# Kernel tuning notes

Measured on AMD Instinct MI355X. Metric: run time of the kernel, lower is better.

## Reference

```python
import jax, jax.numpy as jnp
import numpy as np

EMBED_DIM = 1024
NUM_HEADS = 16
HEAD_DIM = EMBED_DIM // NUM_HEADS
ROPE_BASE = 10000.0


def setup_inputs() -> dict:
    key = jax.random.key(0)
    k1, k2, k3, k4, k5 = jax.random.split(key, 5)
    b, t = 4, 2048
    s = 1.0 / np.sqrt(EMBED_DIM)
    return {
        "query": jax.random.normal(k1, (b, t, EMBED_DIM), jnp.float32),
        "in_proj_w": jax.random.normal(k2, (3 * EMBED_DIM, EMBED_DIM), jnp.float32) * s,
        "in_proj_b": jax.random.normal(k3, (3 * EMBED_DIM,), jnp.float32) * 0.02,
        "out_proj_w": jax.random.normal(k4, (EMBED_DIM, EMBED_DIM), jnp.float32) * s,
        "out_proj_b": jax.random.normal(k5, (EMBED_DIM,), jnp.float32) * 0.02,
    }


def _rope_cos_sin(t: int, dtype):
    inv_freq = 1.0 / (ROPE_BASE ** (jnp.arange(0, HEAD_DIM, 2, dtype=jnp.float32) / HEAD_DIM))
    freqs = jnp.arange(t, dtype=jnp.float32)[:, None] * inv_freq[None, :]  # [t, hd/2]
    return jnp.cos(freqs).astype(dtype), jnp.sin(freqs).astype(dtype)


def _apply_rotary(x, cos, sin):
    # x: [b, h, t, hd]; cos/sin: [t, hd/2]
    x1 = x[..., ::2]
    x2 = x[..., 1::2]
    c = cos[None, None, :, :]
    s = sin[None, None, :, :]
    rotated = jnp.stack((x1 * c - x2 * s, x1 * s + x2 * c), axis=-1)  # [b,h,t,hd/2,2]
    return rotated.reshape(x.shape)


def reference(query, in_proj_w, in_proj_b, out_proj_w, out_proj_b):
    b, t, d = query.shape
    qkv = query @ in_proj_w.T + in_proj_b  # [b, t, 3d]
    q, k, v = jnp.split(qkv, 3, axis=-1)
    def heads(x):
        return x.reshape(b, t, NUM_HEADS, HEAD_DIM).transpose(0, 2, 1, 3)  # [b,h,t,hd]
    q, k, v = heads(q), heads(k), heads(v)
    cos, sin = _rope_cos_sin(t, query.dtype)
    q = _apply_rotary(q, cos, sin)
    k = _apply_rotary(k, cos, sin)
    scale = 1.0 / np.sqrt(HEAD_DIM)
    scores = jnp.einsum('bhqd,bhkd->bhqk', q, k) * scale  # [b,h,t,t]
    probs = jax.nn.softmax(scores, axis=-1)
    attn = jnp.einsum('bhqk,bhkd->bhqd', probs, v)
    out = attn.transpose(0, 2, 1, 3).reshape(b, t, d)
    return out @ out_proj_w.T + out_proj_b
```

## Files before the change

### kernel.cpp

```cpp
#include <hip/hip_runtime.h>
#include <hip/hip_bf16.h>

#define EMBED 1024
#define NHEADS 16
#define HDIM 64
#define BATCH 4
#define SEQ 2048
#define BT (BATCH*SEQ)
#define NQKV (3*EMBED)


typedef _Float16 f16;
typedef __attribute__((ext_vector_type(8))) _Float16 half8;
typedef __attribute__((ext_vector_type(4))) _Float16 half4;
typedef __attribute__((ext_vector_type(2))) __fp16 h2raw;
typedef __attribute__((ext_vector_type(4))) float f32x4;
typedef __attribute__((ext_vector_type(16))) float f32x16;
typedef __attribute__((ext_vector_type(4))) unsigned int u32x4;

#define QSCALE2 0.18033688f

__device__ __forceinline__ float fexp2(float x) {
#if __has_builtin(__builtin_amdgcn_exp2f)
    return __builtin_amdgcn_exp2f(x);
#else
    float r;
    asm("v_exp_f32 %0, %1" : "=v"(r) : "v"(x));
    return r;
#endif
}

__device__ __forceinline__ float fdot2a(unsigned int w, float c) {
#if __has_builtin(__builtin_amdgcn_fdot2)
    h2raw ones;
    ones[0] = (__fp16)1.0f; ones[1] = (__fp16)1.0f;
    return __builtin_amdgcn_fdot2(__builtin_bit_cast(h2raw, w), ones, c, false);
#else
    f16 lo = (f16)__builtin_bit_cast(h2raw, w)[0];
    f16 hi = (f16)__builtin_bit_cast(h2raw, w)[1];
    return c + (float)lo + (float)hi;
#endif
}

__device__ __forceinline__ f32x4 mfma16f(half8 a, half8 b, f32x4 c) {
    return __builtin_amdgcn_mfma_f32_16x16x32_f16(a, b, c, 0, 0, 0);
}
__device__ __forceinline__ f32x16 mfma32(half8 a, half8 b, f32x16 c) {
    return __builtin_amdgcn_mfma_f32_32x32x16_f16(a, b, c, 0, 0, 0);
}
__device__ __forceinline__ f32x16 z16() {
    f32x16 z;
    #pragma unroll
    for (int i = 0; i < 16; i++) z[i] = 0.f;
    return z;
}
__device__ __forceinline__ unsigned int pk16(float a, float b) {
    auto h = __builtin_amdgcn_cvt_pkrtz(a, b);
    return __builtin_bit_cast(unsigned int, h);
}
__device__ __forceinline__ half8 mk8(unsigned int w0, unsigned int w1,
                                     unsigned int w2, unsigned int w3) {
    u32x4 v = (u32x4){w0, w1, w2, w3};
    return __builtin_bit_cast(half8, v);
}
__device__ __forceinline__ void pswap(unsigned int &a, unsigned int &b) {
    asm("v_permlane32_swap_b32 %0, %1" : "+v"(a), "+v"(b));
}

__device__ __forceinline__ half8 cvt8(float4 a, float4 b) {
    half8 r;
    r[0] = (f16)a.x; r[1] = (f16)a.y; r[2] = (f16)a.z; r[3] = (f16)a.w;
    r[4] = (f16)b.x; r[5] = (f16)b.y; r[6] = (f16)b.z; r[7] = (f16)b.w;
    return r;
}

__device__ __forceinline__ void gload16(const void* g, void* l) {
    __builtin_amdgcn_global_load_lds(
        (const __attribute__((address_space(1))) void*)g,
        (__attribute__((address_space(3))) void*)l, 16, 0, 0);
}

__global__ __launch_bounds__(256) void cvt_kernel(
    const float* __restrict__ X, const float* __restrict__ W1,
    const float* __restrict__ W2, f16* __restrict__ Xh,
    f16* __restrict__ W1h, f16* __restrict__ W2h, float2* __restrict__ CSt)
{
    const int u0 = blockIdx.x * 256 + threadIdx.x;
    #pragma unroll
    for (int i = 0; i < 3; i++) {
        const size_t uu = (size_t)u0 + (size_t)i * 524288;
        const float* src; f16* dst; size_t off;
        if (uu < 1048576)      { src = X;  dst = Xh;  off = uu * 8; }
        else if (uu < 1441792) { src = W1; dst = W1h; off = (uu - 1048576) * 8; }
        else                   { src = W2; dst = W2h; off = (uu - 1441792) * 8; }
        float4 a = *(const float4*)(src + off);
        float4 b = *(const float4*)(src + off + 4);
        *(half8*)(dst + off) = cvt8(a, b);
    }
    if (u0 < SEQ * 32) {
        const int t = u0 >> 5, fi = u0 & 31;
        const float ang = (float)t * exp2f(-0.41524103f * (float)fi);
        CSt[u0] = make_float2(cosf(ang), sinf(ang));
    }
}

__global__ __launch_bounds__(512, 4) void qkv_rope_kernel(
    const f16* __restrict__ Xh, const f16* __restrict__ Wh,
    const float* __restrict__ bias, const float2* __restrict__ CSt,
    f16* __restrict__ Qg, f16* __restrict__ Kg, f16* __restrict__ Vtg)
{
    __shared__ __align__(16) char smem[65536];
    f16* A0 = (f16*)smem;
    f16* B0 = (f16*)(smem + 16384);
    f16* A1 = (f16*)(smem + 32768);
    f16* B1 = (f16*)(smem + 49152);
    f16 (*Ep)[136] = (f16(*)[136])smem;

    const int tid = threadIdx.x;

    const int lin = blockIdx.y * 24 + blockIdx.x;
    const int xcd = lin & 7;
    const int c   = lin >> 3;
    const int m0  = (xcd * 8 + (c & 7)) * 128;
    const int n0  = (c >> 3) * 128;

    const int lane = tid & 63;
    const int wv = tid >> 6;
    const int wm = wv >> 2, wn = wv & 3;
    const int quad = lane >> 4, l15 = lane & 15;
    const int sw = (l15 & 7) << 4;

    const int rlo   = tid >> 3;
    const int sslot = (tid & 7) ^ (rlo & 7);
    const f16* asrc = Xh + (size_t)(m0 + rlo) * EMBED + sslot * 8;
    const f16* bsrc = Wh + (size_t)(n0 + rlo) * EMBED + sslot * 8;

    f32x4 acc[4][2];
    #pragma unroll
    for (int i = 0; i < 4; i++)
        #pragma unroll
        for (int j = 0; j < 2; j++) acc[i][j] = (f32x4){0.f,0.f,0.f,0.f};

    gload16(asrc,                      A0 + tid*8);
    gload16(asrc + (size_t)64*EMBED,   A0 + 4096 + tid*8);
    gload16(bsrc,                      B0 + tid*8);
    gload16(bsrc + (size_t)64*EMBED,   B0 + 4096 + tid*8);
    __syncthreads();

    for (int t = 0; t < 16; t++) {
        const f16* Ac = (t & 1) ? A1 : A0;
        const f16* Bc = (t & 1) ? B1 : B0;
        if (t < 15) {
            f16* An = (t & 1) ? A0 : A1;
            f16* Bn = (t & 1) ? B0 : B1;
            const int k0 = (t + 1) * 64;
            gload16(asrc + k0,                    An + tid*8);
            gload16(asrc + (size_t)64*EMBED + k0, An + 4096 + tid*8);
            gload16(bsrc + k0,                    Bn + tid*8);
            gload16(bsrc + (size_t)64*EMBED + k0, Bn + 4096 + tid*8);
        }

        half8 bf[2][2];
        #pragma unroll
        for (int nj = 0; nj < 2; nj++) {
            const int rb = wn*32 + nj*16 + l15;
            bf[nj][0] = *(const half8*)((const char*)Bc + rb*128 + ((quad*16) ^ sw));
            bf[nj][1] = *(const half8*)((const char*)Bc + rb*128 + ((64 + quad*16) ^ sw));
        }
        #pragma unroll
        for (int mi = 0; mi < 4; mi++) {
            const int ra = wm*64 + mi*16 + l15;
            half8 a0 = *(const half8*)((const char*)Ac + ra*128 + ((quad*16) ^ sw));
            half8 a1 = *(const half8*)((const char*)Ac + ra*128 + ((64 + quad*16) ^ sw));
            #pragma unroll
            for (int nj = 0; nj < 2; nj++) {
                acc[mi][nj] = mfma16f(a0, bf[nj][0], acc[mi][nj]);
                acc[mi][nj] = mfma16f(a1, bf[nj][1], acc[mi][nj]);
            }
        }
        __syncthreads();
    }

    const int sect = n0 >> 10;
    const int h0   = (n0 & 1023) >> 6;
    const int bb   = m0 >> 11, t0 = m0 & 2047;

    #pragma unroll
    for (int mi = 0; mi < 4; mi++) {
        #pragma unroll
        for (int nj = 0; nj < 2; nj++) {
            const int ncol = wn*32 + nj*16 + l15;
            const int hd = ncol & 63;
            const float bz = bias[n0 + ncol];
            #pragma unroll
            for (int r = 0; r < 4; r++) {
                const int tl = wm*64 + mi*16 + quad*4 + r;
                float v = acc[mi][nj][r] + bz;
                if (sect < 2) {
                    float partner = __shfl_xor(v, 1, 64);
                    float2 cs2 = CSt[(t0 + tl)*32 + (hd >> 1)];
                    float o = (hd & 1) ? fmaf(partner, cs2.y, v * cs2.x)
                                       : fmaf(v, cs2.x, -(partner * cs2.y));
                    if (sect == 0) o *= QSCALE2;
                    Ep[tl][ncol] = (f16)o;
                } else {
                    Ep[ncol][tl] = (f16)v;
                }
            }
        }
    }
    __syncthreads();

    const int orow = tid >> 2;
    const int oc   = (tid & 3) * 32;
    f16* dst;
    if (sect == 2) {
        const int h = h0 + (orow >> 6), d = orow & 63;
        dst = Vtg + ((size_t)((bb*NHEADS + h) * HDIM + d)) * SEQ + t0 + oc;
    } else {
        const int h = h0 + (oc >> 6);
        f16* base = (sect == 0) ? Qg : Kg;
        dst = base + ((size_t)((bb*NHEADS + h) * SEQ + t0 + orow)) * HDIM + (oc & 63);
    }
    #pragma unroll
    for (int c8 = 0; c8 < 4; c8++)
        *(half8*)(dst + c8*8) = *(const half8*)&Ep[orow][oc + c8*8];
}

__global__ __launch_bounds__(256, 2) void attn_kernel(
    const f16* __restrict__ Qg, const f16* __restrict__ Kg,
    const f16* __restrict__ Vtg, f16* __restrict__ Ow)
{
    __shared__ __align__(16) f16 KV[2][2][64*64];

    const int tid  = threadIdx.x;
    const int lane = tid & 63, wq = tid >> 6;
    const int hi   = lane >> 5, col = lane & 31;

    const int lin = blockIdx.y * 8 + blockIdx.x;
    const int bh  = (lin & 7) + ((lin >> 6) << 3);
    const int qb  = (lin >> 3) & 7;
    const int q0  = qb * 256;

    const f16* Kb = Kg  + (size_t)bh * SEQ * HDIM;
    const f16* Vb = Vtg + (size_t)bh * HDIM * SEQ;

    const int r8   = tid >> 3;
    const int slot = tid & 7;

    #pragma unroll
    for (int g = 0; g < 2; g++) {
        const int row = g*32 + r8;
        const int sc  = (slot ^ (row & 7)) * 8;
        gload16(Kb + (size_t)row * HDIM + sc, &KV[0][0][0] + g*2048 + tid*8);
        gload16(Vb + (size_t)row * SEQ  + sc, &KV[0][1][0] + g*2048 + tid*8);
    }

    half8 qf[2][4];
    #pragma unroll
    for (int nb = 0; nb < 2; nb++) {
        const f16* qsrc = Qg + (size_t)bh * SEQ * HDIM
                        + (size_t)(q0 + wq*64 + nb*32 + col) * HDIM + hi*8;
        #pragma unroll
        for (int kc = 0; kc < 4; kc++)
            qf[nb][kc] = *(const half8*)(qsrc + kc*16);
    }

    f32x16 oacc[2][2];
    oacc[0][0] = z16(); oacc[0][1] = z16();
    oacc[1][0] = z16(); oacc[1][1] = z16();
    float lsA[2] = {0.f, 0.f};
    float lsB[2] = {0.f, 0.f};

    __syncthreads();

    for (int it = 0; it < 32; it++) {
        const f16* kl = &KV[it & 1][0][0];
        const f16* vl = &KV[it & 1][1][0];

        if (it < 31) {
            f16* kd = &KV[(it + 1) & 1][0][0];
            f16* vd = &KV[(it + 1) & 1][1][0];
            const int j0n = (it + 1) * 64;
            #pragma unroll
            for (int g = 0; g < 2; g++) {
                const int row = g*32 + r8;
                const int sc  = (slot ^ (row & 7)) * 8;
                gload16(Kb + (size_t)(j0n + row) * HDIM + sc, kd + g*2048 + tid*8);
                gload16(Vb + (size_t)row * SEQ + j0n + sc,    vd + g*2048 + tid*8);
            }
        }

        half8 kf[2][4];
        #pragma unroll
        for (int jb = 0; jb < 2; jb++) {
            const int row = jb*32 + col;
            const char* base = (const char*)kl + row*128;
            const int sz = (row & 7) << 4;
            #pragma unroll
            for (int kc = 0; kc < 4; kc++)
                kf[jb][kc] = *(const half8*)(base + ((kc*32 + hi*16) ^ sz));
        }

        unsigned int pw[2][4][4];
        #pragma unroll
        for (int nb = 0; nb < 2; nb++) {
            f32x16 s0 = z16(), s1 = z16();
            __builtin_amdgcn_s_setprio(1);
            #pragma unroll
            for (int kc = 0; kc < 4; kc++) s0 = mfma32(kf[0][kc], qf[nb][kc], s0);
            #pragma unroll
            for (int kc = 0; kc < 4; kc++) s1 = mfma32(kf[1][kc], qf[nb][kc], s1);
            __builtin_amdgcn_s_setprio(0);

            float e0[16], e1[16];
            #pragma unroll
            for (int r = 0; r < 16; r++) {
                e0[r] = fexp2(s0[r]);
                e1[r] = fexp2(s1[r]);
            }

            unsigned int a, b;
            a = pk16(e0[0],  e0[1]);  b = pk16(e0[4],  e0[5]);
            lsA[nb] = fdot2a(a, lsA[nb]); lsB[nb] = fdot2a(b, lsB[nb]);
            pswap(a, b); pw[nb][0][0] = a; pw[nb][0][2] = b;
            a = pk16(e0[2],  e0[3]);  b = pk16(e0[6],  e0[7]);
            lsA[nb] = fdot2a(a, lsA[nb]); lsB[nb] = fdot2a(b, lsB[nb]);
            pswap(a, b); pw[nb][0][1] = a; pw[nb][0][3] = b;
            a = pk16(e0[8],  e0[9]);  b = pk16(e0[12], e0[13]);
            lsA[nb] = fdot2a(a, lsA[nb]); lsB[nb] = fdot2a(b, lsB[nb]);
            pswap(a, b); pw[nb][1][0] = a; pw[nb][1][2] = b;
            a = pk16(e0[10], e0[11]); b = pk16(e0[14], e0[15]);
            lsA[nb] = fdot2a(a, lsA[nb]); lsB[nb] = fdot2a(b, lsB[nb]);
            pswap(a, b); pw[nb][1][1] = a; pw[nb][1][3] = b;

            a = pk16(e1[0],  e1[1]);  b = pk16(e1[4],  e1[5]);
            lsA[nb] = fdot2a(a, lsA[nb]); lsB[nb] = fdot2a(b, lsB[nb]);
            pswap(a, b); pw[nb][2][0] = a; pw[nb][2][2] = b;
            a = pk16(e1[2],  e1[3]);  b = pk16(e1[6],  e1[7]);
            lsA[nb] = fdot2a(a, lsA[nb]); lsB[nb] = fdot2a(b, lsB[nb]);
            pswap(a, b); pw[nb][2][1] = a; pw[nb][2][3] = b;
            a = pk16(e1[8],  e1[9]);  b = pk16(e1[12], e1[13]);
            lsA[nb] = fdot2a(a, lsA[nb]); lsB[nb] = fdot2a(b, lsB[nb]);
            pswap(a, b); pw[nb][3][0] = a; pw[nb][3][2] = b;
            a = pk16(e1[10], e1[11]); b = pk16(e1[14], e1[15]);
            lsA[nb] = fdot2a(a, lsA[nb]); lsB[nb] = fdot2a(b, lsB[nb]);
            pswap(a, b); pw[nb][3][1] = a; pw[nb][3][3] = b;
        }

        __builtin_amdgcn_s_setprio(1);
        #pragma unroll
        for (int kc2 = 0; kc2 < 4; kc2++) {
            half8 pb0 = mk8(pw[0][kc2][0], pw[0][kc2][1], pw[0][kc2][2], pw[0][kc2][3]);
            half8 pb1 = mk8(pw[1][kc2][0], pw[1][kc2][1], pw[1][kc2][2], pw[1][kc2][3]);
            #pragma unroll
            for (int db = 0; db < 2; db++) {
                const int row = db*32 + col;
                const int sz = (row & 7) << 4;
                half8 vf = *(const half8*)((const char*)vl + row*128
                                           + ((kc2*32 + hi*16) ^ sz));
                oacc[db][0] = mfma32(vf, pb0, oacc[db][0]);
                oacc[db][1] = mfma32(vf, pb1, oacc[db][1]);
            }
        }
        __builtin_amdgcn_s_setprio(0);

        __syncthreads();
    }

    float invl[2];
    {
        float l0 = lsA[0] + lsB[0];
        float l1 = lsA[1] + lsB[1];
        invl[0] = 1.0f / (l0 + __shfl_xor(l0, 32, 64));
        invl[1] = 1.0f / (l1 + __shfl_xor(l1, 32, 64));
    }

    const int bb = bh >> 4, h = bh & 15;
    #pragma unroll
    for (int nb = 0; nb < 2; nb++) {
        const int t = q0 + wq*64 + nb*32 + col;
        f16* od = Ow + (size_t)(bb*SEQ + t) * EMBED + h*HDIM + hi*4;
        #pragma unroll
        for (int db = 0; db < 2; db++) {
            #pragma unroll
            for (int rg = 0; rg < 4; rg++) {
                half4 o;
                o[0] = (f16)(oacc[db][nb][rg*4+0] * invl[nb]);
                o[1] = (f16)(oacc[db][nb][rg*4+1] * invl[nb]);
                o[2] = (f16)(oacc[db][nb][rg*4+2] * invl[nb]);
                o[3] = (f16)(oacc[db][nb][rg*4+3] * invl[nb]);
                *(half4*)(od + db*32 + rg*8) = o;
            }
        }
    }
}

__global__ __launch_bounds__(512, 4) void outproj_kernel(
    const f16* __restrict__ Aw, const f16* __restrict__ Wh,
    const float* __restrict__ bias, float* __restrict__ Out)
{
    __shared__ __align__(16) char smem[65536];
    f16* A0 = (f16*)smem;
    f16* B0 = (f16*)(smem + 16384);
    f16* A1 = (f16*)(smem + 32768);
    f16* B1 = (f16*)(smem + 49152);

    const int tid = threadIdx.x;

    const int lin = blockIdx.y * 8 + blockIdx.x;
    const int xcd = lin & 7;
    const int c   = lin >> 3;
    const int m0  = (xcd * 8 + (c & 7)) * 128;
    const int n0  = (c >> 3) * 128;

    const int lane = tid & 63;
    const int wv = tid >> 6;
    const int wm = wv >> 2, wn = wv & 3;
    const int quad = lane >> 4, l15 = lane & 15;
    const int sw = (l15 & 7) << 4;

    const int rlo   = tid >> 3;
    const int sslot = (tid & 7) ^ (rlo & 7);
    const f16* asrc = Aw + (size_t)(m0 + rlo) * EMBED + sslot * 8;
    const f16* bsrc = Wh + (size_t)(n0 + rlo) * EMBED + sslot * 8;

    f32x4 acc[4][2];
    #pragma unroll
    for (int i = 0; i < 4; i++)
        #pragma unroll
        for (int j = 0; j < 2; j++) acc[i][j] = (f32x4){0.f,0.f,0.f,0.f};

    gload16(asrc,                      A0 + tid*8);
    gload16(asrc + (size_t)64*EMBED,   A0 + 4096 + tid*8);
    gload16(bsrc,                      B0 + tid*8);
    gload16(bsrc + (size_t)64*EMBED,   B0 + 4096 + tid*8);
    __syncthreads();

    for (int t = 0; t < 16; t++) {
        const f16* Ac = (t & 1) ? A1 : A0;
        const f16* Bc = (t & 1) ? B1 : B0;
        if (t < 15) {
            f16* An = (t & 1) ? A0 : A1;
            f16* Bn = (t & 1) ? B0 : B1;
            const int k0 = (t + 1) * 64;
            gload16(asrc + k0,                    An + tid*8);
            gload16(asrc + (size_t)64*EMBED + k0, An + 4096 + tid*8);
            gload16(bsrc + k0,                    Bn + tid*8);
            gload16(bsrc + (size_t)64*EMBED + k0, Bn + 4096 + tid*8);
        }

        half8 bf[2][2];
        #pragma unroll
        for (int nj = 0; nj < 2; nj++) {
            const int rb = wn*32 + nj*16 + l15;
            bf[nj][0] = *(const half8*)((const char*)Bc + rb*128 + ((quad*16) ^ sw));
            bf[nj][1] = *(const half8*)((const char*)Bc + rb*128 + ((64 + quad*16) ^ sw));
        }
        #pragma unroll
        for (int mi = 0; mi < 4; mi++) {
            const int ra = wm*64 + mi*16 + l15;
            half8 a0 = *(const half8*)((const char*)Ac + ra*128 + ((quad*16) ^ sw));
            half8 a1 = *(const half8*)((const char*)Ac + ra*128 + ((64 + quad*16) ^ sw));
            #pragma unroll
            for (int nj = 0; nj < 2; nj++) {
                acc[mi][nj] = mfma16f(a0, bf[nj][0], acc[mi][nj]);
                acc[mi][nj] = mfma16f(a1, bf[nj][1], acc[mi][nj]);
            }
        }
        __syncthreads();
    }

    #pragma unroll
    for (int mi = 0; mi < 4; mi++) {
        #pragma unroll
        for (int nj = 0; nj < 2; nj++) {
            const int n = n0 + wn*32 + nj*16 + l15;
            const float bz = bias[n];
            #pragma unroll
            for (int r = 0; r < 4; r++) {
                const int m = m0 + wm*64 + mi*16 + quad*4 + r;
                Out[(size_t)m * EMBED + n] = acc[mi][nj][r] + bz;
            }
        }
    }
}

extern "C" void kernel_launch(void* const* d_in, const int* in_sizes, int n_in,
                              void* d_out, int out_size, void* d_ws, size_t ws_size,
                              hipStream_t stream)
{
    const float* query = (const float*)d_in[0];
    const float* in_w  = (const float*)d_in[1];
    const float* in_b  = (const float*)d_in[2];
    const float* out_w = (const float*)d_in[3];
    const float* out_b = (const float*)d_in[4];
    float* out = (float*)d_out;

    const size_t NT = (size_t)BATCH * NHEADS * SEQ * HDIM;
    char* ws = (char*)d_ws;
    f16* Qg  = (f16*)ws;
    f16* Kg  = (f16*)(ws + 2*NT);
    f16* Vtg = (f16*)(ws + 4*NT);
    f16* Aw  = (f16*)(ws + 6*NT);
    f16* Xh  = (f16*)(ws + 6*NT);
    f16* W1h = (f16*)(ws + 8*NT);
    f16* W2h = (f16*)(ws + 8*NT + 6291456);
    float2* CSt = (float2*)(ws + 8*NT + 6291456 + 2097152);

    cvt_kernel<<<2048, 256, 0, stream>>>(query, in_w, out_w, Xh, W1h, W2h, CSt);
    dim3 g1(NQKV / 128, BT / 128);
    qkv_rope_kernel<<<g1, 512, 0, stream>>>(Xh, W1h, in_b, CSt, Qg, Kg, Vtg);
    dim3 g2(SEQ / 256, BATCH * NHEADS);
    attn_kernel<<<g2, 256, 0, stream>>>(Qg, Kg, Vtg, Aw);
    dim3 g3(EMBED / 128, BT / 128);
    outproj_kernel<<<g3, 512, 0, stream>>>(Aw, W2h, out_b, out);
}
```

Measured before the change: 290.4 us.

## Switch projection GEMMs to 32x32 MFMA with 4 waves and single-buffered LDS

Both projection GEMMs (QKV+RoPE and output) move from 8-wave blocks issuing 16x16x32 MFMAs to 4-wave blocks where each wave computes a 64x64 tile with 32x32x16 MFMAs. The LDS double buffer is dropped in favour of one A/B buffer loaded and consumed each k-step, and the epilogue and store indexing are remapped to the 32x32 accumulator layout. Larger MFMA tiles cut LDS fragment reads per flop and the smaller LDS footprint may allow more resident blocks. The cost is that global-load latency is no longer overlapped with compute within a block.

Measured after the change: 279.2 us. 1.04x faster.

```diff
diff --git a/kernel.cpp b/kernel.cpp
--- a/kernel.cpp
+++ b/kernel.cpp
@@ -42,9 +42,6 @@
 #endif
 }
 
-__device__ __forceinline__ f32x4 mfma16f(half8 a, half8 b, f32x4 c) {
-    return __builtin_amdgcn_mfma_f32_16x16x32_f16(a, b, c, 0, 0, 0);
-}
 __device__ __forceinline__ f32x16 mfma32(half8 a, half8 b, f32x16 c) {
     return __builtin_amdgcn_mfma_f32_32x32x16_f16(a, b, c, 0, 0, 0);
 }
@@ -104,16 +101,14 @@
     }
 }
 
-__global__ __launch_bounds__(512, 4) void qkv_rope_kernel(
+__global__ __launch_bounds__(256, 4) void qkv_rope_kernel(
     const f16* __restrict__ Xh, const f16* __restrict__ Wh,
     const float* __restrict__ bias, const float2* __restrict__ CSt,
     f16* __restrict__ Qg, f16* __restrict__ Kg, f16* __restrict__ Vtg)
 {
-    __shared__ __align__(16) char smem[65536];
-    f16* A0 = (f16*)smem;
-    f16* B0 = (f16*)(smem + 16384);
-    f16* A1 = (f16*)(smem + 32768);
-    f16* B1 = (f16*)(smem + 49152);
+    __shared__ __align__(16) char smem[34816];
+    f16* Ah = (f16*)smem;
+    f16* Bh = (f16*)(smem + 16384);
     f16 (*Ep)[136] = (f16(*)[136])smem;
 
     const int tid = threadIdx.x;
@@ -126,57 +121,42 @@
 
     const int lane = tid & 63;
     const int wv = tid >> 6;
-    const int wm = wv >> 2, wn = wv & 3;
-    const int quad = lane >> 4, l15 = lane & 15;
-    const int sw = (l15 & 7) << 4;
+    const int wm = wv >> 1, wn = wv & 1;
+    const int hi = lane >> 5, col = lane & 31;
 
     const int rlo   = tid >> 3;
     const int sslot = (tid & 7) ^ (rlo & 7);
     const f16* asrc = Xh + (size_t)(m0 + rlo) * EMBED + sslot * 8;
     const f16* bsrc = Wh + (size_t)(n0 + rlo) * EMBED + sslot * 8;
 
-    f32x4 acc[4][2];
-    #pragma unroll
-    for (int i = 0; i < 4; i++)
-        #pragma unroll
-        for (int j = 0; j < 2; j++) acc[i][j] = (f32x4){0.f,0.f,0.f,0.f};
-
-    gload16(asrc,                      A0 + tid*8);
-    gload16(asrc + (size_t)64*EMBED,   A0 + 4096 + tid*8);
-    gload16(bsrc,                      B0 + tid*8);
-    gload16(bsrc + (size_t)64*EMBED,   B0 + 4096 + tid*8);
-    __syncthreads();
-
-    for (int t = 0; t < 16; t++) {
-        const f16* Ac = (t & 1) ? A1 : A0;
-        const f16* Bc = (t & 1) ? B1 : B0;
-        if (t < 15) {
-            f16* An = (t & 1) ? A0 : A1;
-            f16* Bn = (t & 1) ? B0 : B1;
-            const int k0 = (t + 1) * 64;
-            gload16(asrc + k0,                    An + tid*8);
-            gload16(asrc + (size_t)64*EMBED + k0, An + 4096 + tid*8);
-            gload16(bsrc + k0,                    Bn + tid*8);
-            gload16(bsrc + (size_t)64*EMBED + k0, Bn + 4096 + tid*8);
-        }
-
-        half8 bf[2][2];
-        #pragma unroll
-        for (int nj = 0; nj < 2; nj++) {
-            const int rb = wn*32 + nj*16 + l15;
-            bf[nj][0] = *(const half8*)((const char*)Bc + rb*128 + ((quad*16) ^ sw));
-            bf[nj][1] = *(const half8*)((const char*)Bc + rb*128 + ((64 + quad*16) ^ sw));
-        }
-        #pragma unroll
-        for (int mi = 0; mi < 4; mi++) {
-            const int ra = wm*64 + mi*16 + l15;
-            half8 a0 = *(const half8*)((const char*)Ac + ra*128 + ((quad*16) ^ sw));
-            half8 a1 = *(const half8*)((const char*)Ac + ra*128 + ((64 + quad*16) ^ sw));
-            #pragma unroll
-            for (int nj = 0; nj < 2; nj++) {
-                acc[mi][nj] = mfma16f(a0, bf[nj][0], acc[mi][nj]);
-                acc[mi][nj] = mfma16f(a1, bf[nj][1], acc[mi][nj]);
-            }
+    const int ra0 = wm*64 + col,      ra1 = wm*64 + 32 + col;
+    const int rb0 = wn*64 + col,      rb1 = wn*64 + 32 + col;
+    const int sza0 = (ra0 & 7) << 4,  sza1 = (ra1 & 7) << 4;
+    const int szb0 = (rb0 & 7) << 4,  szb1 = (rb1 & 7) << 4;
+
+    f32x16 acc[2][2];
+    acc[0][0] = z16(); acc[0][1] = z16();
+    acc[1][0] = z16(); acc[1][1] = z16();
+
+    for (int k0 = 0; k0 < EMBED; k0 += 64) {
+        #pragma unroll
+        for (int i = 0; i < 4; i++) {
+            gload16(asrc + (size_t)i*32*EMBED + k0, Ah + i*2048 + tid*8);
+            gload16(bsrc + (size_t)i*32*EMBED + k0, Bh + i*2048 + tid*8);
+        }
+        __syncthreads();
+
+        #pragma unroll
+        for (int ks = 0; ks < 4; ks++) {
+            const int ko = ks*32 + hi*16;
+            half8 a0 = *(const half8*)((const char*)Ah + ra0*128 + (ko ^ sza0));
+            half8 a1 = *(const half8*)((const char*)Ah + ra1*128 + (ko ^ sza1));
+            half8 b0 = *(const half8*)((const char*)Bh + rb0*128 + (ko ^ szb0));
+            half8 b1 = *(const half8*)((const char*)Bh + rb1*128 + (ko ^ szb1));
+            acc[0][0] = mfma32(a0, b0, acc[0][0]);
+            acc[0][1] = mfma32(a0, b1, acc[0][1]);
+            acc[1][0] = mfma32(a1, b0, acc[1][0]);
+            acc[1][1] = mfma32(a1, b1, acc[1][1]);
         }
         __syncthreads();
     }
@@ -186,16 +166,16 @@
     const int bb   = m0 >> 11, t0 = m0 & 2047;
 
     #pragma unroll
-    for (int mi = 0; mi < 4; mi++) {
-        #pragma unroll
-        for (int nj = 0; nj < 2; nj++) {
-            const int ncol = wn*32 + nj*16 + l15;
+    for (int mb = 0; mb < 2; mb++) {
+        #pragma unroll
+        for (int nbk = 0; nbk < 2; nbk++) {
+            const int ncol = wn*64 + nbk*32 + col;
             const int hd = ncol & 63;
             const float bz = bias[n0 + ncol];
             #pragma unroll
-            for (int r = 0; r < 4; r++) {
-                const int tl = wm*64 + mi*16 + quad*4 + r;
-                float v = acc[mi][nj][r] + bz;
+            for (int reg = 0; reg < 16; reg++) {
+                const int tl = wm*64 + mb*32 + (reg & 3) + 8*(reg >> 2) + 4*hi;
+                float v = acc[mb][nbk][reg] + bz;
                 if (sect < 2) {
                     float partner = __shfl_xor(v, 1, 64);
                     float2 cs2 = CSt[(t0 + tl)*32 + (hd >> 1)];
@@ -211,19 +191,19 @@
     }
     __syncthreads();
 
-    const int orow = tid >> 2;
-    const int oc   = (tid & 3) * 32;
+    const int orow = tid >> 1;
+    const int oc   = (tid & 1) * 64;
     f16* dst;
     if (sect == 2) {
         const int h = h0 + (orow >> 6), d = orow & 63;
         dst = Vtg + ((size_t)((bb*NHEADS + h) * HDIM + d)) * SEQ + t0 + oc;
     } else {
-        const int h = h0 + (oc >> 6);
+        const int h = h0 + (tid & 1);
         f16* base = (sect == 0) ? Qg : Kg;
-        dst = base + ((size_t)((bb*NHEADS + h) * SEQ + t0 + orow)) * HDIM + (oc & 63);
-    }
-    #pragma unroll
-    for (int c8 = 0; c8 < 4; c8++)
+        dst = base + ((size_t)((bb*NHEADS + h) * SEQ + t0 + orow)) * HDIM;
+    }
+    #pragma unroll
+    for (int c8 = 0; c8 < 8; c8++)
         *(half8*)(dst + c8*8) = *(const half8*)&Ep[orow][oc + c8*8];
 }
 
@@ -396,15 +376,13 @@
     }
 }
 
-__global__ __launch_bounds__(512, 4) void outproj_kernel(
+__global__ __launch_bounds__(256, 4) void outproj_kernel(
     const f16* __restrict__ Aw, const f16* __restrict__ Wh,
     const float* __restrict__ bias, float* __restrict__ Out)
 {
-    __shared__ __align__(16) char smem[65536];
-    f16* A0 = (f16*)smem;
-    f16* B0 = (f16*)(smem + 16384);
-    f16* A1 = (f16*)(smem + 32768);
-    f16* B1 = (f16*)(smem + 49152);
+    __shared__ __align__(16) char smem[32768];
+    f16* Ah = (f16*)smem;
+    f16* Bh = (f16*)(smem + 16384);
 
     const int tid = threadIdx.x;
 
@@ -416,71 +394,56 @@
 
     const int lane = tid & 63;
     const int wv = tid >> 6;
-    const int wm = wv >> 2, wn = wv & 3;
-    const int quad = lane >> 4, l15 = lane & 15;
-    const int sw = (l15 & 7) << 4;
+    const int wm = wv >> 1, wn = wv & 1;
+    const int hi = lane >> 5, col = lane & 31;
 
     const int rlo   = tid >> 3;
     const int sslot = (tid & 7) ^ (rlo & 7);
     const f16* asrc = Aw + (size_t)(m0 + rlo) * EMBED + sslot * 8;
     const f16* bsrc = Wh + (size_t)(n0 + rlo) * EMBED + sslot * 8;
 
-    f32x4 acc[4][2];
-    #pragma unroll
-    for (int i = 0; i < 4; i++)
-        #pragma unroll
-        for (int j = 0; j < 2; j++) acc[i][j] = (f32x4){0.f,0.f,0.f,0.f};
-
-    gload16(asrc,                      A0 + tid*8);
-    gload16(asrc + (size_t)64*EMBED,   A0 + 4096 + tid*8);
-    gload16(bsrc,                      B0 + tid*8);
-    gload16(bsrc + (size_t)64*EMBED,   B0 + 4096 + tid*8);
-    __syncthreads();
-
-    for (int t = 0; t < 16; t++) {
-        const f16* Ac = (t & 1) ? A1 : A0;
-        const f16* Bc = (t & 1) ? B1 : B0;
-        if (t < 15) {
-            f16* An = (t & 1) ? A0 : A1;
-            f16* Bn = (t & 1) ? B0 : B1;
-            const int k0 = (t + 1) * 64;
-            gload16(asrc + k0,                    An + tid*8);
-            gload16(asrc + (size_t)64*EMBED + k0, An + 4096 + tid*8);
-            gload16(bsrc + k0,                    Bn + tid*8);
-            gload16(bsrc + (size_t)64*EMBED + k0, Bn + 4096 + tid*8);
-        }
-
-        half8 bf[2][2];
-        #pragma unroll
-        for (int nj = 0; nj < 2; nj++) {
-            const int rb = wn*32 + nj*16 + l15;
-            bf[nj][0] = *(const half8*)((const char*)Bc + rb*128 + ((quad*16) ^ sw));
-            bf[nj][1] = *(const half8*)((const char*)Bc + rb*128 + ((64 + quad*16) ^ sw));
-        }
-        #pragma unroll
-        for (int mi = 0; mi < 4; mi++) {
-            const int ra = wm*64 + mi*16 + l15;
-            half8 a0 = *(const half8*)((const char*)Ac + ra*128 + ((quad*16) ^ sw));
-            half8 a1 = *(const half8*)((const char*)Ac + ra*128 + ((64 + quad*16) ^ sw));
-            #pragma unroll
-            for (int nj = 0; nj < 2; nj++) {
-                acc[mi][nj] = mfma16f(a0, bf[nj][0], acc[mi][nj]);
-                acc[mi][nj] = mfma16f(a1, bf[nj][1], acc[mi][nj]);
-            }
+    const int ra0 = wm*64 + col,      ra1 = wm*64 + 32 + col;
+    const int rb0 = wn*64 + col,      rb1 = wn*64 + 32 + col;
+    const int sza0 = (ra0 & 7) << 4,  sza1 = (ra1 & 7) << 4;
+    const int szb0 = (rb0 & 7) << 4,  szb1 = (rb1 & 7) << 4;
+
+    f32x16 acc[2][2];
+    acc[0][0] = z16(); acc[0][1] = z16();
+    acc[1][0] = z16(); acc[1][1] = z16();
+
+    for (int k0 = 0; k0 < EMBED; k0 += 64) {
+        #pragma unroll
+        for (int i = 0; i < 4; i++) {
+            gload16(asrc + (size_t)i*32*EMBED + k0, Ah + i*2048 + tid*8);
+            gload16(bsrc + (size_t)i*32*EMBED + k0, Bh + i*2048 + tid*8);
         }
         __syncthreads();
-    }
-
-    #pragma unroll
-    for (int mi = 0; mi < 4; mi++) {
-        #pragma unroll
-        for (int nj = 0; nj < 2; nj++) {
-            const int n = n0 + wn*32 + nj*16 + l15;
+
+        #pragma unroll
+        for (int ks = 0; ks < 4; ks++) {
+            const int ko = ks*32 + hi*16;
+            half8 a0 = *(const half8*)((const char*)Ah + ra0*128 + (ko ^ sza0));
+            half8 a1 = *(const half8*)((const char*)Ah + ra1*128 + (ko ^ sza1));
+            half8 b0 = *(const half8*)((const char*)Bh + rb0*128 + (ko ^ szb0));
+            half8 b1 = *(const half8*)((const char*)Bh + rb1*128 + (ko ^ szb1));
+            acc[0][0] = mfma32(a0, b0, acc[0][0]);
+            acc[0][1] = mfma32(a0, b1, acc[0][1]);
+            acc[1][0] = mfma32(a1, b0, acc[1][0]);
+            acc[1][1] = mfma32(a1, b1, acc[1][1]);
+        }
+        __syncthreads();
+    }
+
+    #pragma unroll
+    for (int mb = 0; mb < 2; mb++) {
+        #pragma unroll
+        for (int nbk = 0; nbk < 2; nbk++) {
+            const int n = n0 + wn*64 + nbk*32 + col;
             const float bz = bias[n];
             #pragma unroll
-            for (int r = 0; r < 4; r++) {
-                const int m = m0 + wm*64 + mi*16 + quad*4 + r;
-                Out[(size_t)m * EMBED + n] = acc[mi][nj][r] + bz;
+            for (int reg = 0; reg < 16; reg++) {
+                const int m = m0 + wm*64 + mb*32 + (reg & 3) + 8*(reg >> 2) + 4*hi;
+                Out[(size_t)m * EMBED + n] = acc[mb][nbk][reg] + bz;
             }
         }
     }
@@ -510,9 +473,9 @@
 
     cvt_kernel<<<2048, 256, 0, stream>>>(query, in_w, out_w, Xh, W1h, W2h, CSt);
     dim3 g1(NQKV / 128, BT / 128);
-    qkv_rope_kernel<<<g1, 512, 0, stream>>>(Xh, W1h, in_b, CSt, Qg, Kg, Vtg);
+    qkv_rope_kernel<<<g1, 256, 0, stream>>>(Xh, W1h, in_b, CSt, Qg, Kg, Vtg);
     dim3 g2(SEQ / 256, BATCH * NHEADS);
     attn_kernel<<<g2, 256, 0, stream>>>(Qg, Kg, Vtg, Aw);
     dim3 g3(EMBED / 128, BT / 128);
-    outproj_kernel<<<g3, 512, 0, stream>>>(Aw, W2h, out_b, out);
-}
+    outproj_kernel<<<g3, 256, 0, stream>>>(Aw, W2h, out_b, out);
+}
```
